# Kernel optimization log

Hardware: AMD Instinct MI355X
Metric: run time of the kernel (lower is better)

Reference implementation:

```python
import jax, jax.numpy as jnp
import numpy as np

EPS = 1e-5  # torch LayerNorm default eps
L2_EPS = 1e-12


def _l2norm(t, axis=-1):
    return t / jnp.sqrt(jnp.sum(t * t, axis=axis, keepdims=True) + L2_EPS)


def setup_inputs() -> dict:
    key = jax.random.key(0)
    k1, k2, k3 = jax.random.split(key, 3)
    b, n, d = 4, 2048, 1024
    h, e, cs = 8, 16, 2048
    x = jax.random.normal(k1, (b, n, d), dtype=jnp.float32)
    # xavier_normal_ on [h, d, e]: fan_in = d*e, fan_out = h*e
    std = float(np.sqrt(2.0 / (d * e + h * e)))
    rand_projs = jax.random.normal(k2, (h, d, e), dtype=jnp.float32) * std
    codebook = jax.random.normal(k3, (h, cs, e), dtype=jnp.float32)
    return {"x": x, "rand_projs": rand_projs, "codebook": codebook}


def reference(x, rand_projs, codebook):
    # LayerNorm over last dim, no affine
    mu = jnp.mean(x, axis=-1, keepdims=True)
    var = jnp.mean((x - mu) ** 2, axis=-1, keepdims=True)
    xn = (x - mu) / jnp.sqrt(var + EPS)
    # per-head random projection: [b,n,d] x [h,d,e] -> [b,n,h,e]
    proj = jnp.einsum('bnd,hde->bnhe', xn, rand_projs)
    # cosine-sim VQ per head: normalize both, argmax similarity
    q = _l2norm(proj, axis=-1)                 # [b,n,h,e]
    cb = _l2norm(codebook, axis=-1)            # [h,c,e]
    sim = jnp.einsum('bnhe,hce->bnhc', q, cb)  # [b,n,h,c]
    indices = jnp.argmax(sim, axis=-1)         # [b,n,h] int
    return indices
```

## Files before the change

kernel.cpp:

```cpp
#include <hip/hip_runtime.h>
#include <math.h>


typedef short bf16x8 __attribute__((ext_vector_type(8)));
typedef float f32x4 __attribute__((ext_vector_type(4)));

__device__ __forceinline__ void stage16(const float* g, float* lds_base) {
  __builtin_amdgcn_global_load_lds(
      (const __attribute__((address_space(1))) void*)g,
      (__attribute__((address_space(3))) void*)lds_base, 16, 0, 0);
}

__device__ __forceinline__ unsigned short f2bf(float f) {
  unsigned u = __builtin_bit_cast(unsigned, f);
  unsigned r = (u + 0x7FFFu + ((u >> 16) & 1u)) >> 16;
  return (unsigned short)r;
}
__device__ __forceinline__ float bf2f(unsigned short b) {
  return __builtin_bit_cast(float, (unsigned)b << 16);
}
__device__ __forceinline__ void split3(float v, unsigned short& h,
                                       unsigned short& m, unsigned short& l) {
  h = f2bf(v);
  float r = v - bf2f(h);
  m = f2bf(r);
  float r2 = r - bf2f(m);
  l = f2bf(r2);
}

__global__ __launch_bounds__(256) void k_prep(const float* __restrict__ cb,
                                              const float* __restrict__ W,
                                              unsigned short* __restrict__ cfrag,
                                              float* __restrict__ csum,
                                              unsigned short* __restrict__ wfrag) {
  __shared__ float red[16][17];
  const int bid = blockIdx.x;
  const int t = threadIdx.x;
  if (bid < 64) {
    int v = bid * 256 + t;
    int h = v >> 11, c = v & 2047, tl = c >> 4, n = c & 15;
    const float4* p = (const float4*)(cb + (size_t)v * 16);
    float4 q0 = p[0], q1 = p[1], q2 = p[2], q3 = p[3];
    float f[16] = {q0.x,q0.y,q0.z,q0.w, q1.x,q1.y,q1.z,q1.w,
                   q2.x,q2.y,q2.z,q2.w, q3.x,q3.y,q3.z,q3.w};
    double s = 0.0;
#pragma unroll
    for (int i = 0; i < 16; ++i) s += (double)f[i] * (double)f[i];
    double inv = 1.0 / sqrt(s + 1e-12);
    __attribute__((aligned(16))) unsigned short vp[3][16];
#pragma unroll
    for (int i = 0; i < 16; ++i)
      split3((float)((double)f[i] * inv), vp[0][i], vp[1][i], vp[2][i]);
#pragma unroll
    for (int pp = 0; pp < 3; ++pp) {
      size_t base = ((((size_t)h * 128 + tl) * 3 + pp) * 16 + n) * 16;
      ((bf16x8*)(cfrag + base))[0] = ((bf16x8*)vp[pp])[0];
      ((bf16x8*)(cfrag + base))[1] = ((bf16x8*)vp[pp])[1];
    }
  } else if (bid < 72) {
    int h = bid - 64;
    int e = t & 15, part = t >> 4;
    const float* base = W + h * 16384 + e;
    float s = 0.f;
    int d0 = part * 64;
    for (int i = 0; i < 64; ++i) s += base[(d0 + i) * 16];
    red[e][part] = s;
    __syncthreads();
    if (t < 16) {
      float tt = 0.f;
#pragma unroll
      for (int p = 0; p < 16; ++p) tt += red[t][p];
      csum[h * 16 + t] = tt;
    }
  } else {
    int id = (bid - 72) * 256 + t;
    int o = id & 1, n = (id >> 1) & 15, c = (id >> 5) & 7, dg = id >> 8;
    __attribute__((aligned(16))) unsigned short vp[3][8];
#pragma unroll
    for (int j = 0; j < 8; ++j) {
      float v = W[c * 16384 + (dg * 16 + o * 8 + j) * 16 + n];
      split3(v, vp[0][j], vp[1][j], vp[2][j]);
    }
#pragma unroll
    for (int pp = 0; pp < 3; ++pp) {
      size_t base = ((((size_t)dg * 8 + c) * 3 + pp) * 16 + n) * 16 + o * 8;
      *(bf16x8*)(wfrag + base) = *(bf16x8*)vp[pp];
    }
  }
}

__global__ __launch_bounds__(512) void k_proj(const float* __restrict__ x,
                                              const unsigned short* __restrict__ wfrag,
                                              const float* __restrict__ csum,
                                              unsigned short* __restrict__ ph,
                                              unsigned short* __restrict__ pm,
                                              unsigned short* __restrict__ pl) {
  __shared__ __align__(16) float smem[16 * 1028];
  __shared__ float sPs[8][2][16];
  __shared__ float sMu[16];
  const int t = threadIdx.x;
  const int lane = t & 63, w = t >> 6;
  const int r0 = blockIdx.x * 16;
  const int q = lane >> 4, n16 = lane & 15, oct = q & 1;
  const bool qlt2 = (q < 2);
  const int p1 = qlt2 ? 0 : 1, p2 = qlt2 ? 1 : 0, p3 = qlt2 ? 2 : 0;

#pragma unroll
  for (int rr = 0; rr < 2; ++rr)
#pragma unroll
    for (int j4 = 0; j4 < 4; ++j4)
      stage16(x + (size_t)(r0 + 2 * w + rr) * 1024 + j4 * 256 + lane * 4,
              smem + (2 * w + rr) * 1028 + j4 * 256);
  __syncthreads();

  f32x4 acc[8];
#pragma unroll
  for (int h = 0; h < 8; ++h) acc[h] = (f32x4){0.f, 0.f, 0.f, 0.f};
  float ps = 0.f;

#pragma unroll 4
  for (int dg2 = 0; dg2 < 8; ++dg2) {
    const int dg = w * 8 + dg2;
    const int dq = dg * 16 + oct * 8;
    float4 xa = *(const float4*)(smem + n16 * 1028 + dq);
    float4 xb = *(const float4*)(smem + n16 * 1028 + dq + 4);
    float xf[8] = {xa.x, xa.y, xa.z, xa.w, xb.x, xb.y, xb.z, xb.w};
    ps += ((xf[0] + xf[1]) + (xf[2] + xf[3])) +
          ((xf[4] + xf[5]) + (xf[6] + xf[7]));
    __attribute__((aligned(16))) unsigned short s1[8], s3[8];
#pragma unroll
    for (int j = 0; j < 8; ++j) {
      unsigned short hh, mm, ll;
      split3(xf[j], hh, mm, ll);
      s1[j] = qlt2 ? hh : mm;
      s3[j] = qlt2 ? hh : ll;
    }
    bf16x8 a1 = *(bf16x8*)s1;
    bf16x8 a3 = *(bf16x8*)s3;
#pragma unroll
    for (int hh = 0; hh < 8; ++hh) {
      size_t b0 = (((size_t)(dg * 8 + hh) * 3) * 16 + n16) * 16 + oct * 8;
      bf16x8 b1 = *(const bf16x8*)(wfrag + b0 + p1 * 256);
      bf16x8 b2 = *(const bf16x8*)(wfrag + b0 + p2 * 256);
      bf16x8 b3 = *(const bf16x8*)(wfrag + b0 + p3 * 256);
      acc[hh] = __builtin_amdgcn_mfma_f32_16x16x32_bf16(a1, b1, acc[hh], 0, 0, 0);
      acc[hh] = __builtin_amdgcn_mfma_f32_16x16x32_bf16(a1, b2, acc[hh], 0, 0, 0);
      acc[hh] = __builtin_amdgcn_mfma_f32_16x16x32_bf16(a3, b3, acc[hh], 0, 0, 0);
    }
  }

  __syncthreads();
  float* sAcc = smem;

  if (w >= 4) {
#pragma unroll
    for (int hh = 0; hh < 8; ++hh)
#pragma unroll
      for (int r = 0; r < 4; ++r)
        sAcc[((w - 4) * 64 + lane) * 33 + hh * 4 + r] = acc[hh][r];
  }
  if (q < 2) sPs[w][q][n16] = ps;
  __syncthreads();
  if (w < 4) {
#pragma unroll
    for (int hh = 0; hh < 8; ++hh)
#pragma unroll
      for (int r = 0; r < 4; ++r)
        sAcc[(w * 64 + lane) * 33 + hh * 4 + r] =
            acc[hh][r] + sAcc[(w * 64 + lane) * 33 + hh * 4 + r];
  }
  if (t < 16) {
    float s = 0.f;
#pragma unroll
    for (int w2 = 0; w2 < 8; ++w2) s += sPs[w2][0][t] + sPs[w2][1][t];
    sMu[t] = s * (1.0f / 1024.0f);
  }
  __syncthreads();

  const int l = t & 63, head = t >> 6;
  const int lq = l >> 4, ln = l & 15;
  const float cs = csum[head * 16 + ln];
#pragma unroll
  for (int r = 0; r < 4; ++r) {
    const int f = head * 4 + r;
    float v = ((sAcc[(0 * 64 + l) * 33 + f] + sAcc[(1 * 64 + l) * 33 + f]) +
               (sAcc[(2 * 64 + l) * 33 + f] + sAcc[(3 * 64 + l) * 33 + f]));
    const int row16 = lq * 4 + r;
    float tv = v - sMu[row16] * cs;
    unsigned short vh, vm, vl;
    split3(tv, vh, vm, vl);
    size_t base = ((size_t)head * 8192 + r0 + row16) * 16 + ln;
    ph[base] = vh; pm[base] = vm; pl[base] = vl;
  }
}

__global__ __launch_bounds__(256) void k_argmax(
    const unsigned short* __restrict__ ph, const unsigned short* __restrict__ pm,
    const unsigned short* __restrict__ pl, const unsigned short* __restrict__ cfrag,
    float* __restrict__ amv, int* __restrict__ ami) {
  __shared__ __align__(16) unsigned short sB[12288];
  const int t = threadIdx.x;
  const int lane = t & 63, w = t >> 6;
  const int h = blockIdx.y;
  const int z = blockIdx.z;
  const int r0 = blockIdx.x * 256 + w * 64;
  const int q = lane >> 4, n16 = lane & 15;
  const int ehalf = (q & 1) * 8;
  const bool qlt2 = (q < 2);
  const int p1 = qlt2 ? 0 : 1, p2 = qlt2 ? 1 : 0, p3 = qlt2 ? 2 : 0;

  const float* src = (const float*)(cfrag + ((size_t)(h * 128 + z * 16) * 3) * 256);
#pragma unroll
  for (int i = 0; i < 6; ++i)
    stage16(src + ((size_t)((i * 4 + w) * 64) + lane) * 4,
            (float*)sB + (i * 4 + w) * 256);

  const unsigned short* pa1 = qlt2 ? ph : pm;
  const unsigned short* pa3 = qlt2 ? ph : pl;
  bf16x8 a1[4], a3[4];
#pragma unroll
  for (int rt = 0; rt < 4; ++rt) {
    size_t off = ((size_t)h * 8192 + r0 + rt * 16 + n16) * 16 + ehalf;
    a1[rt] = *(const bf16x8*)(pa1 + off);
    a3[rt] = *(const bf16x8*)(pa3 + off);
  }

  float best[4][4];
  int   bidx[4][4];
#pragma unroll
  for (int rt = 0; rt < 4; ++rt)
#pragma unroll
    for (int r = 0; r < 4; ++r) { best[rt][r] = -3.402823466e38f; bidx[rt][r] = 0; }

  __syncthreads();

  for (int tile = 0; tile < 16; ++tile) {
    const int b0 = tile * 768 + n16 * 16 + ehalf;
    bf16x8 b1 = *(const bf16x8*)(sB + b0 + p1 * 256);
    bf16x8 b2 = *(const bf16x8*)(sB + b0 + p2 * 256);
    bf16x8 b3 = *(const bf16x8*)(sB + b0 + p3 * 256);
    const int code = z * 256 + tile * 16 + n16;
#pragma unroll
    for (int rt = 0; rt < 4; ++rt) {
      f32x4 acc = {0.f, 0.f, 0.f, 0.f};
      acc = __builtin_amdgcn_mfma_f32_16x16x32_bf16(a1[rt], b1, acc, 0, 0, 0);
      acc = __builtin_amdgcn_mfma_f32_16x16x32_bf16(a1[rt], b2, acc, 0, 0, 0);
      acc = __builtin_amdgcn_mfma_f32_16x16x32_bf16(a3[rt], b3, acc, 0, 0, 0);
#pragma unroll
      for (int r = 0; r < 4; ++r)
        if (acc[r] > best[rt][r]) { best[rt][r] = acc[r]; bidx[rt][r] = code; }
    }
  }

#pragma unroll
  for (int off = 8; off >= 1; off >>= 1) {
#pragma unroll
    for (int rt = 0; rt < 4; ++rt)
#pragma unroll
      for (int r = 0; r < 4; ++r) {
        float ov = __shfl_xor(best[rt][r], off, 16);
        int   oi = __shfl_xor(bidx[rt][r], off, 16);
        if (ov > best[rt][r] || (ov == best[rt][r] && oi < bidx[rt][r])) {
          best[rt][r] = ov; bidx[rt][r] = oi;
        }
      }
  }
  if (n16 == 0) {
#pragma unroll
    for (int rt = 0; rt < 4; ++rt)
#pragma unroll
      for (int r = 0; r < 4; ++r) {
        int row = r0 + rt * 16 + q * 4 + r;
        size_t o = (size_t)z * 65536 + (size_t)row * 8 + h;
        amv[o] = best[rt][r]; ami[o] = bidx[rt][r];
      }
  }
}

__global__ __launch_bounds__(256) void k_amred(const float* __restrict__ amv,
                                               const int* __restrict__ ami,
                                               int* __restrict__ out) {
  int i = blockIdx.x * 256 + threadIdx.x;
  float bv = amv[i]; int bi = ami[i];
#pragma unroll
  for (int z = 1; z < 8; ++z) {
    float v = amv[(size_t)z * 65536 + i];
    if (v > bv) { bv = v; bi = ami[(size_t)z * 65536 + i]; }
  }
  out[i] = bi;
}

extern "C" void kernel_launch(void* const* d_in, const int* in_sizes, int n_in,
                              void* d_out, int out_size, void* d_ws, size_t ws_size,
                              hipStream_t stream) {
  (void)in_sizes; (void)n_in; (void)out_size; (void)ws_size;
  const float* x  = (const float*)d_in[0];
  const float* rp = (const float*)d_in[1];
  const float* cb = (const float*)d_in[2];
  int* out = (int*)d_out;

  float* ws = (float*)d_ws;
  float*          csum  = ws;
  float*          amv   = ws + 128;
  int*            ami   = (int*)(ws + 524416);
  unsigned short* wfrag = (unsigned short*)(ws + 1048704);
  unsigned short* cfrag = (unsigned short*)(ws + 1245312);
  unsigned short* ph    = (unsigned short*)(ws + 1638528);
  unsigned short* pm    = (unsigned short*)(ws + 2162816);
  unsigned short* pl    = (unsigned short*)(ws + 2687104);

  hipLaunchKernelGGL(k_prep,    dim3(136),       dim3(256), 0, stream, cb, rp, cfrag, csum, wfrag);
  hipLaunchKernelGGL(k_proj,    dim3(512),       dim3(512), 0, stream, x, wfrag, csum, ph, pm, pl);
  hipLaunchKernelGGL(k_argmax,  dim3(32, 8, 8),  dim3(256), 0, stream, ph, pm, pl, cfrag, amv, ami);
  hipLaunchKernelGGL(k_amred,   dim3(256),       dim3(256), 0, stream, amv, ami, out);
}
```

Before: 144.3 us.

## Fuse all four stages into one persistent kernel with grid barriers

Merges prep, projection, argmax and reduction into a single 512-block kernel, separating the stages with software grid-wide barriers built on atomics. The argmax stage is remapped so each block runs two half-block work items per rep over two reps, with each 4-wave group using its own LDS slice. This is meant to remove three kernel launch gaps and the tail idle time between them. In exchange it adds a memset launch, spin-wait barrier cost, and a deadlock risk if all 512 blocks cannot be co-resident, and prep work now runs on only one thread in eight.

```diff
diff --git a/kernel.cpp b/kernel.cpp
--- a/kernel.cpp
+++ b/kernel.cpp
@@ -28,17 +28,48 @@
   l = f2bf(r2);
 }
 
-__global__ __launch_bounds__(256) void k_prep(const float* __restrict__ cb,
-                                              const float* __restrict__ W,
-                                              unsigned short* __restrict__ cfrag,
-                                              float* __restrict__ csum,
-                                              unsigned short* __restrict__ wfrag) {
-  __shared__ float red[16][17];
+__device__ __forceinline__ void gbar(unsigned* cnt, unsigned* flag,
+                                     unsigned nb) {
+  __syncthreads();
+  if (threadIdx.x == 0) {
+    __threadfence();
+    unsigned prev = __hip_atomic_fetch_add(cnt, 1u, __ATOMIC_ACQ_REL,
+                                           __HIP_MEMORY_SCOPE_AGENT);
+    if (prev == nb - 1) {
+      __hip_atomic_store(flag, 1u, __ATOMIC_RELEASE,
+                         __HIP_MEMORY_SCOPE_AGENT);
+    } else {
+      while (__hip_atomic_load(flag, __ATOMIC_ACQUIRE,
+                               __HIP_MEMORY_SCOPE_AGENT) == 0u)
+        __builtin_amdgcn_s_sleep(1);
+    }
+    __threadfence();
+  }
+  __syncthreads();
+}
+
+__global__ __launch_bounds__(512, 4) void k_all(
+    const float* __restrict__ x, const float* __restrict__ W,
+    const float* __restrict__ cb, int* __restrict__ out,
+    float* __restrict__ csum, float* __restrict__ amv, int* __restrict__ ami,
+    unsigned short* __restrict__ wfrag, unsigned short* __restrict__ cfrag,
+    unsigned short* __restrict__ ph, unsigned short* __restrict__ pm,
+    unsigned short* __restrict__ pl, unsigned* __restrict__ bar) {
+  __shared__ __align__(16) float smemF[16 * 1028];
+  __shared__ float sPs[8][2][16];
+  __shared__ float sMu[16];
+
   const int bid = blockIdx.x;
   const int t = threadIdx.x;
-  if (bid < 64) {
-    int v = bid * 256 + t;
-    int h = v >> 11, c = v & 2047, tl = c >> 4, n = c & 15;
+  const int tid = bid * 512 + t;
+  const int lane = t & 63, w = t >> 6;
+  const int q = lane >> 4, n16 = lane & 15, oct = q & 1;
+  const bool qlt2 = (q < 2);
+  const int p1 = qlt2 ? 0 : 1, p2 = qlt2 ? 1 : 0, p3 = qlt2 ? 2 : 0;
+
+  if (tid < 131072 && (tid & 7) == 0) {
+    int v = tid >> 3;
+    int hh = v >> 11, c = v & 2047, tl = c >> 4, n = c & 15;
     const float4* p = (const float4*)(cb + (size_t)v * 16);
     float4 q0 = p[0], q1 = p[1], q2 = p[2], q3 = p[3];
     float f[16] = {q0.x,q0.y,q0.z,q0.w, q1.x,q1.y,q1.z,q1.w,
@@ -53,27 +84,12 @@
       split3((float)((double)f[i] * inv), vp[0][i], vp[1][i], vp[2][i]);
 #pragma unroll
     for (int pp = 0; pp < 3; ++pp) {
-      size_t base = ((((size_t)h * 128 + tl) * 3 + pp) * 16 + n) * 16;
+      size_t base = ((((size_t)hh * 128 + tl) * 3 + pp) * 16 + n) * 16;
       ((bf16x8*)(cfrag + base))[0] = ((bf16x8*)vp[pp])[0];
       ((bf16x8*)(cfrag + base))[1] = ((bf16x8*)vp[pp])[1];
     }
-  } else if (bid < 72) {
-    int h = bid - 64;
-    int e = t & 15, part = t >> 4;
-    const float* base = W + h * 16384 + e;
-    float s = 0.f;
-    int d0 = part * 64;
-    for (int i = 0; i < 64; ++i) s += base[(d0 + i) * 16];
-    red[e][part] = s;
-    __syncthreads();
-    if (t < 16) {
-      float tt = 0.f;
-#pragma unroll
-      for (int p = 0; p < 16; ++p) tt += red[t][p];
-      csum[h * 16 + t] = tt;
-    }
-  } else {
-    int id = (bid - 72) * 256 + t;
+  } else if (tid >= 131072 && (tid & 7) == 0) {
+    int id = (tid - 131072) >> 3;
     int o = id & 1, n = (id >> 1) & 15, c = (id >> 5) & 7, dg = id >> 8;
     __attribute__((aligned(16))) unsigned short vp[3][8];
 #pragma unroll
@@ -87,207 +103,216 @@
       *(bf16x8*)(wfrag + base) = *(bf16x8*)vp[pp];
     }
   }
-}
-
-__global__ __launch_bounds__(512) void k_proj(const float* __restrict__ x,
-                                              const unsigned short* __restrict__ wfrag,
-                                              const float* __restrict__ csum,
-                                              unsigned short* __restrict__ ph,
-                                              unsigned short* __restrict__ pm,
-                                              unsigned short* __restrict__ pl) {
-  __shared__ __align__(16) float smem[16 * 1028];
-  __shared__ float sPs[8][2][16];
-  __shared__ float sMu[16];
-  const int t = threadIdx.x;
-  const int lane = t & 63, w = t >> 6;
-  const int r0 = blockIdx.x * 16;
-  const int q = lane >> 4, n16 = lane & 15, oct = q & 1;
-  const bool qlt2 = (q < 2);
-  const int p1 = qlt2 ? 0 : 1, p2 = qlt2 ? 1 : 0, p3 = qlt2 ? 2 : 0;
-
-#pragma unroll
-  for (int rr = 0; rr < 2; ++rr)
-#pragma unroll
-    for (int j4 = 0; j4 < 4; ++j4)
-      stage16(x + (size_t)(r0 + 2 * w + rr) * 1024 + j4 * 256 + lane * 4,
-              smem + (2 * w + rr) * 1028 + j4 * 256);
-  __syncthreads();
-
-  f32x4 acc[8];
-#pragma unroll
-  for (int h = 0; h < 8; ++h) acc[h] = (f32x4){0.f, 0.f, 0.f, 0.f};
-  float ps = 0.f;
+  if (bid >= 504) {
+    float (*red)[17] = (float(*)[17])smemF;
+    int hh = bid - 504;
+    if (t < 256) {
+      int e = t & 15, part = t >> 4;
+      const float* base = W + hh * 16384 + e;
+      float s = 0.f;
+      int d0 = part * 64;
+      for (int i = 0; i < 64; ++i) s += base[(d0 + i) * 16];
+      red[e][part] = s;
+    }
+    __syncthreads();
+    if (t < 16) {
+      float tt = 0.f;
+#pragma unroll
+      for (int p = 0; p < 16; ++p) tt += red[t][p];
+      csum[hh * 16 + t] = tt;
+    }
+  }
+
+  gbar(bar + 0, bar + 1, gridDim.x);
+
+  {
+    const int r0 = bid * 16;
+#pragma unroll
+    for (int rr = 0; rr < 2; ++rr)
+#pragma unroll
+      for (int j4 = 0; j4 < 4; ++j4)
+        stage16(x + (size_t)(r0 + 2 * w + rr) * 1024 + j4 * 256 + lane * 4,
+                smemF + (2 * w + rr) * 1028 + j4 * 256);
+    __syncthreads();
+
+    f32x4 acc[8];
+#pragma unroll
+    for (int h = 0; h < 8; ++h) acc[h] = (f32x4){0.f, 0.f, 0.f, 0.f};
+    float ps = 0.f;
 
 #pragma unroll 4
-  for (int dg2 = 0; dg2 < 8; ++dg2) {
-    const int dg = w * 8 + dg2;
-    const int dq = dg * 16 + oct * 8;
-    float4 xa = *(const float4*)(smem + n16 * 1028 + dq);
-    float4 xb = *(const float4*)(smem + n16 * 1028 + dq + 4);
-    float xf[8] = {xa.x, xa.y, xa.z, xa.w, xb.x, xb.y, xb.z, xb.w};
-    ps += ((xf[0] + xf[1]) + (xf[2] + xf[3])) +
-          ((xf[4] + xf[5]) + (xf[6] + xf[7]));
-    __attribute__((aligned(16))) unsigned short s1[8], s3[8];
-#pragma unroll
-    for (int j = 0; j < 8; ++j) {
-      unsigned short hh, mm, ll;
-      split3(xf[j], hh, mm, ll);
-      s1[j] = qlt2 ? hh : mm;
-      s3[j] = qlt2 ? hh : ll;
-    }
-    bf16x8 a1 = *(bf16x8*)s1;
-    bf16x8 a3 = *(bf16x8*)s3;
-#pragma unroll
-    for (int hh = 0; hh < 8; ++hh) {
-      size_t b0 = (((size_t)(dg * 8 + hh) * 3) * 16 + n16) * 16 + oct * 8;
-      bf16x8 b1 = *(const bf16x8*)(wfrag + b0 + p1 * 256);
-      bf16x8 b2 = *(const bf16x8*)(wfrag + b0 + p2 * 256);
-      bf16x8 b3 = *(const bf16x8*)(wfrag + b0 + p3 * 256);
-      acc[hh] = __builtin_amdgcn_mfma_f32_16x16x32_bf16(a1, b1, acc[hh], 0, 0, 0);
-      acc[hh] = __builtin_amdgcn_mfma_f32_16x16x32_bf16(a1, b2, acc[hh], 0, 0, 0);
-      acc[hh] = __builtin_amdgcn_mfma_f32_16x16x32_bf16(a3, b3, acc[hh], 0, 0, 0);
-    }
-  }
-
-  __syncthreads();
-  float* sAcc = smem;
-
-  if (w >= 4) {
-#pragma unroll
-    for (int hh = 0; hh < 8; ++hh)
-#pragma unroll
-      for (int r = 0; r < 4; ++r)
-        sAcc[((w - 4) * 64 + lane) * 33 + hh * 4 + r] = acc[hh][r];
-  }
-  if (q < 2) sPs[w][q][n16] = ps;
-  __syncthreads();
-  if (w < 4) {
-#pragma unroll
-    for (int hh = 0; hh < 8; ++hh)
-#pragma unroll
-      for (int r = 0; r < 4; ++r)
-        sAcc[(w * 64 + lane) * 33 + hh * 4 + r] =
-            acc[hh][r] + sAcc[(w * 64 + lane) * 33 + hh * 4 + r];
-  }
-  if (t < 16) {
-    float s = 0.f;
-#pragma unroll
-    for (int w2 = 0; w2 < 8; ++w2) s += sPs[w2][0][t] + sPs[w2][1][t];
-    sMu[t] = s * (1.0f / 1024.0f);
-  }
-  __syncthreads();
-
-  const int l = t & 63, head = t >> 6;
-  const int lq = l >> 4, ln = l & 15;
-  const float cs = csum[head * 16 + ln];
-#pragma unroll
-  for (int r = 0; r < 4; ++r) {
-    const int f = head * 4 + r;
-    float v = ((sAcc[(0 * 64 + l) * 33 + f] + sAcc[(1 * 64 + l) * 33 + f]) +
-               (sAcc[(2 * 64 + l) * 33 + f] + sAcc[(3 * 64 + l) * 33 + f]));
-    const int row16 = lq * 4 + r;
-    float tv = v - sMu[row16] * cs;
-    unsigned short vh, vm, vl;
-    split3(tv, vh, vm, vl);
-    size_t base = ((size_t)head * 8192 + r0 + row16) * 16 + ln;
-    ph[base] = vh; pm[base] = vm; pl[base] = vl;
-  }
-}
-
-__global__ __launch_bounds__(256) void k_argmax(
-    const unsigned short* __restrict__ ph, const unsigned short* __restrict__ pm,
-    const unsigned short* __restrict__ pl, const unsigned short* __restrict__ cfrag,
-    float* __restrict__ amv, int* __restrict__ ami) {
-  __shared__ __align__(16) unsigned short sB[12288];
-  const int t = threadIdx.x;
-  const int lane = t & 63, w = t >> 6;
-  const int h = blockIdx.y;
-  const int z = blockIdx.z;
-  const int r0 = blockIdx.x * 256 + w * 64;
-  const int q = lane >> 4, n16 = lane & 15;
-  const int ehalf = (q & 1) * 8;
-  const bool qlt2 = (q < 2);
-  const int p1 = qlt2 ? 0 : 1, p2 = qlt2 ? 1 : 0, p3 = qlt2 ? 2 : 0;
-
-  const float* src = (const float*)(cfrag + ((size_t)(h * 128 + z * 16) * 3) * 256);
-#pragma unroll
-  for (int i = 0; i < 6; ++i)
-    stage16(src + ((size_t)((i * 4 + w) * 64) + lane) * 4,
-            (float*)sB + (i * 4 + w) * 256);
-
-  const unsigned short* pa1 = qlt2 ? ph : pm;
-  const unsigned short* pa3 = qlt2 ? ph : pl;
-  bf16x8 a1[4], a3[4];
-#pragma unroll
-  for (int rt = 0; rt < 4; ++rt) {
-    size_t off = ((size_t)h * 8192 + r0 + rt * 16 + n16) * 16 + ehalf;
-    a1[rt] = *(const bf16x8*)(pa1 + off);
-    a3[rt] = *(const bf16x8*)(pa3 + off);
-  }
-
-  float best[4][4];
-  int   bidx[4][4];
-#pragma unroll
-  for (int rt = 0; rt < 4; ++rt)
-#pragma unroll
-    for (int r = 0; r < 4; ++r) { best[rt][r] = -3.402823466e38f; bidx[rt][r] = 0; }
-
-  __syncthreads();
-
-  for (int tile = 0; tile < 16; ++tile) {
-    const int b0 = tile * 768 + n16 * 16 + ehalf;
-    bf16x8 b1 = *(const bf16x8*)(sB + b0 + p1 * 256);
-    bf16x8 b2 = *(const bf16x8*)(sB + b0 + p2 * 256);
-    bf16x8 b3 = *(const bf16x8*)(sB + b0 + p3 * 256);
-    const int code = z * 256 + tile * 16 + n16;
-#pragma unroll
-    for (int rt = 0; rt < 4; ++rt) {
-      f32x4 acc = {0.f, 0.f, 0.f, 0.f};
-      acc = __builtin_amdgcn_mfma_f32_16x16x32_bf16(a1[rt], b1, acc, 0, 0, 0);
-      acc = __builtin_amdgcn_mfma_f32_16x16x32_bf16(a1[rt], b2, acc, 0, 0, 0);
-      acc = __builtin_amdgcn_mfma_f32_16x16x32_bf16(a3[rt], b3, acc, 0, 0, 0);
-#pragma unroll
-      for (int r = 0; r < 4; ++r)
-        if (acc[r] > best[rt][r]) { best[rt][r] = acc[r]; bidx[rt][r] = code; }
-    }
-  }
-
-#pragma unroll
-  for (int off = 8; off >= 1; off >>= 1) {
-#pragma unroll
-    for (int rt = 0; rt < 4; ++rt)
-#pragma unroll
-      for (int r = 0; r < 4; ++r) {
-        float ov = __shfl_xor(best[rt][r], off, 16);
-        int   oi = __shfl_xor(bidx[rt][r], off, 16);
-        if (ov > best[rt][r] || (ov == best[rt][r] && oi < bidx[rt][r])) {
-          best[rt][r] = ov; bidx[rt][r] = oi;
+    for (int dg2 = 0; dg2 < 8; ++dg2) {
+      const int dg = w * 8 + dg2;
+      const int dq = dg * 16 + oct * 8;
+      float4 xa = *(const float4*)(smemF + n16 * 1028 + dq);
+      float4 xb = *(const float4*)(smemF + n16 * 1028 + dq + 4);
+      float xf[8] = {xa.x, xa.y, xa.z, xa.w, xb.x, xb.y, xb.z, xb.w};
+      ps += ((xf[0] + xf[1]) + (xf[2] + xf[3])) +
+            ((xf[4] + xf[5]) + (xf[6] + xf[7]));
+      __attribute__((aligned(16))) unsigned short s1[8], s3[8];
+#pragma unroll
+      for (int j = 0; j < 8; ++j) {
+        unsigned short hh, mm, ll;
+        split3(xf[j], hh, mm, ll);
+        s1[j] = qlt2 ? hh : mm;
+        s3[j] = qlt2 ? hh : ll;
+      }
+      bf16x8 a1 = *(bf16x8*)s1;
+      bf16x8 a3 = *(bf16x8*)s3;
+#pragma unroll
+      for (int hh = 0; hh < 8; ++hh) {
+        size_t b0 = (((size_t)(dg * 8 + hh) * 3) * 16 + n16) * 16 + oct * 8;
+        bf16x8 b1 = *(const bf16x8*)(wfrag + b0 + p1 * 256);
+        bf16x8 b2 = *(const bf16x8*)(wfrag + b0 + p2 * 256);
+        bf16x8 b3 = *(const bf16x8*)(wfrag + b0 + p3 * 256);
+        acc[hh] = __builtin_amdgcn_mfma_f32_16x16x32_bf16(a1, b1, acc[hh], 0, 0, 0);
+        acc[hh] = __builtin_amdgcn_mfma_f32_16x16x32_bf16(a1, b2, acc[hh], 0, 0, 0);
+        acc[hh] = __builtin_amdgcn_mfma_f32_16x16x32_bf16(a3, b3, acc[hh], 0, 0, 0);
+      }
+    }
+
+    __syncthreads();
+    float* sAcc = smemF;
+
+    if (w >= 4) {
+#pragma unroll
+      for (int hh = 0; hh < 8; ++hh)
+#pragma unroll
+        for (int r = 0; r < 4; ++r)
+          sAcc[((w - 4) * 64 + lane) * 33 + hh * 4 + r] = acc[hh][r];
+    }
+    if (q < 2) sPs[w][q][n16] = ps;
+    __syncthreads();
+    if (w < 4) {
+#pragma unroll
+      for (int hh = 0; hh < 8; ++hh)
+#pragma unroll
+        for (int r = 0; r < 4; ++r)
+          sAcc[(w * 64 + lane) * 33 + hh * 4 + r] =
+              acc[hh][r] + sAcc[(w * 64 + lane) * 33 + hh * 4 + r];
+    }
+    if (t < 16) {
+      float s = 0.f;
+#pragma unroll
+      for (int w2 = 0; w2 < 8; ++w2) s += sPs[w2][0][t] + sPs[w2][1][t];
+      sMu[t] = s * (1.0f / 1024.0f);
+    }
+    __syncthreads();
+
+    const int l = t & 63, head = t >> 6;
+    const int lq = l >> 4, ln = l & 15;
+    const float cs = csum[head * 16 + ln];
+#pragma unroll
+    for (int r = 0; r < 4; ++r) {
+      const int f = head * 4 + r;
+      float v = ((sAcc[(0 * 64 + l) * 33 + f] + sAcc[(1 * 64 + l) * 33 + f]) +
+                 (sAcc[(2 * 64 + l) * 33 + f] + sAcc[(3 * 64 + l) * 33 + f]));
+      const int row16 = lq * 4 + r;
+      float tv = v - sMu[row16] * cs;
+      unsigned short vh, vm, vl;
+      split3(tv, vh, vm, vl);
+      size_t base = ((size_t)head * 8192 + r0 + row16) * 16 + ln;
+      ph[base] = vh; pm[base] = vm; pl[base] = vl;
+    }
+  }
+
+  gbar(bar + 2, bar + 3, gridDim.x);
+
+  {
+    unsigned short* sB = (unsigned short*)smemF;
+    const int wg = w >> 2, lw = w & 3;
+    const int ehalf = oct * 8;
+    const unsigned short* pa1 = qlt2 ? ph : pm;
+    const unsigned short* pa3 = qlt2 ? ph : pl;
+    unsigned short* sBw = sB + wg * 12288;
+
+    for (int rep = 0; rep < 2; ++rep) {
+      const int lid = rep * 1024 + bid * 2 + wg;
+      const int z = lid & 7, h = (lid >> 3) & 7, rg = lid >> 6;
+      const int r0 = rg * 256 + lw * 64;
+
+      __syncthreads();
+      const float* src =
+          (const float*)(cfrag + ((size_t)(h * 128 + z * 16) * 3) * 256);
+#pragma unroll
+      for (int i = 0; i < 6; ++i)
+        stage16(src + ((size_t)((i * 4 + lw) * 64) + lane) * 4,
+                (float*)sBw + (i * 4 + lw) * 256);
+
+      bf16x8 a1[4], a3[4];
+#pragma unroll
+      for (int rt = 0; rt < 4; ++rt) {
+        size_t off = ((size_t)h * 8192 + r0 + rt * 16 + n16) * 16 + ehalf;
+        a1[rt] = *(const bf16x8*)(pa1 + off);
+        a3[rt] = *(const bf16x8*)(pa3 + off);
+      }
+
+      float best[4][4];
+      int bidx[4][4];
+#pragma unroll
+      for (int rt = 0; rt < 4; ++rt)
+#pragma unroll
+        for (int r = 0; r < 4; ++r) {
+          best[rt][r] = -3.402823466e38f; bidx[rt][r] = 0;
         }
-      }
-  }
-  if (n16 == 0) {
-#pragma unroll
-    for (int rt = 0; rt < 4; ++rt)
-#pragma unroll
-      for (int r = 0; r < 4; ++r) {
-        int row = r0 + rt * 16 + q * 4 + r;
-        size_t o = (size_t)z * 65536 + (size_t)row * 8 + h;
-        amv[o] = best[rt][r]; ami[o] = bidx[rt][r];
-      }
-  }
-}
-
-__global__ __launch_bounds__(256) void k_amred(const float* __restrict__ amv,
-                                               const int* __restrict__ ami,
-                                               int* __restrict__ out) {
-  int i = blockIdx.x * 256 + threadIdx.x;
-  float bv = amv[i]; int bi = ami[i];
-#pragma unroll
-  for (int z = 1; z < 8; ++z) {
-    float v = amv[(size_t)z * 65536 + i];
-    if (v > bv) { bv = v; bi = ami[(size_t)z * 65536 + i]; }
-  }
-  out[i] = bi;
+
+      __syncthreads();
+
+      for (int tile = 0; tile < 16; ++tile) {
+        const int b0 = tile * 768 + n16 * 16 + ehalf;
+        bf16x8 b1 = *(const bf16x8*)(sBw + b0 + p1 * 256);
+        bf16x8 b2 = *(const bf16x8*)(sBw + b0 + p2 * 256);
+        bf16x8 b3 = *(const bf16x8*)(sBw + b0 + p3 * 256);
+        const int code = z * 256 + tile * 16 + n16;
+#pragma unroll
+        for (int rt = 0; rt < 4; ++rt) {
+          f32x4 acc = {0.f, 0.f, 0.f, 0.f};
+          acc = __builtin_amdgcn_mfma_f32_16x16x32_bf16(a1[rt], b1, acc, 0, 0, 0);
+          acc = __builtin_amdgcn_mfma_f32_16x16x32_bf16(a1[rt], b2, acc, 0, 0, 0);
+          acc = __builtin_amdgcn_mfma_f32_16x16x32_bf16(a3[rt], b3, acc, 0, 0, 0);
+#pragma unroll
+          for (int r = 0; r < 4; ++r)
+            if (acc[r] > best[rt][r]) { best[rt][r] = acc[r]; bidx[rt][r] = code; }
+        }
+      }
+
+#pragma unroll
+      for (int off = 8; off >= 1; off >>= 1) {
+#pragma unroll
+        for (int rt = 0; rt < 4; ++rt)
+#pragma unroll
+          for (int r = 0; r < 4; ++r) {
+            float ov = __shfl_xor(best[rt][r], off, 16);
+            int oi = __shfl_xor(bidx[rt][r], off, 16);
+            if (ov > best[rt][r] || (ov == best[rt][r] && oi < bidx[rt][r])) {
+              best[rt][r] = ov; bidx[rt][r] = oi;
+            }
+          }
+      }
+      if (n16 == 0) {
+#pragma unroll
+        for (int rt = 0; rt < 4; ++rt)
+#pragma unroll
+          for (int r = 0; r < 4; ++r) {
+            int row = r0 + rt * 16 + q * 4 + r;
+            size_t o = (size_t)z * 65536 + (size_t)row * 8 + h;
+            amv[o] = best[rt][r]; ami[o] = bidx[rt][r];
+          }
+      }
+    }
+  }
+
+  gbar(bar + 4, bar + 5, gridDim.x);
+
+  if (tid < 65536) {
+    float bv = amv[tid]; int bi = ami[tid];
+#pragma unroll
+    for (int z = 1; z < 8; ++z) {
+      float v = amv[(size_t)z * 65536 + tid];
+      if (v > bv) { bv = v; bi = ami[(size_t)z * 65536 + tid]; }
+    }
+    out[tid] = bi;
+  }
 }
 
 extern "C" void kernel_launch(void* const* d_in, const int* in_sizes, int n_in,
@@ -308,9 +333,10 @@
   unsigned short* ph    = (unsigned short*)(ws + 1638528);
   unsigned short* pm    = (unsigned short*)(ws + 2162816);
   unsigned short* pl    = (unsigned short*)(ws + 2687104);
-
-  hipLaunchKernelGGL(k_prep,    dim3(136),       dim3(256), 0, stream, cb, rp, cfrag, csum, wfrag);
-  hipLaunchKernelGGL(k_proj,    dim3(512),       dim3(512), 0, stream, x, wfrag, csum, ph, pm, pl);
-  hipLaunchKernelGGL(k_argmax,  dim3(32, 8, 8),  dim3(256), 0, stream, ph, pm, pl, cfrag, amv, ami);
-  hipLaunchKernelGGL(k_amred,   dim3(256),       dim3(256), 0, stream, amv, ami, out);
-}
+  unsigned*       bar   = (unsigned*)(ws + 3211392);
+
+  hipMemsetAsync((void*)bar, 0, 6 * sizeof(unsigned), stream);
+  hipLaunchKernelGGL(k_all, dim3(512), dim3(512), 0, stream,
+                     x, rp, cb, out, csum, amv, ami, wfrag, cfrag,
+                     ph, pm, pl, bar);
+}
```

Result: slower. 374.4 us (+159.4%).

## Fuse projection, codebook argmax and reduction into one kernel

Applied to the files above, without the earlier changes.

Merges the projection kernel, the split-codebook argmax kernel and the cross-split reduction kernel into a single kernel. The split bf16 projections stay in LDS instead of going through global memory, and each wave scans the full 2048-entry codebook for one head, reading codebook fragments straight from global/L2. This drops two launches and the intermediate global traffic. In exchange only 512 blocks run the argmax with a long serial loop over 128 tiles per wave, reading codebook fragments from global memory with no LDS staging, so parallelism drops.

```diff
diff --git a/kernel.cpp b/kernel.cpp
--- a/kernel.cpp
+++ b/kernel.cpp
@@ -89,13 +89,12 @@
   }
 }
 
-__global__ __launch_bounds__(512) void k_proj(const float* __restrict__ x,
+__global__ __launch_bounds__(512) void k_main(const float* __restrict__ x,
                                               const unsigned short* __restrict__ wfrag,
+                                              const unsigned short* __restrict__ cfrag,
                                               const float* __restrict__ csum,
-                                              unsigned short* __restrict__ ph,
-                                              unsigned short* __restrict__ pm,
-                                              unsigned short* __restrict__ pl) {
-  __shared__ __align__(16) float smem[16 * 1028];
+                                              int* __restrict__ out) {
+  __shared__ __align__(16) float smemF[16 * 1028];
   __shared__ float sPs[8][2][16];
   __shared__ float sMu[16];
   const int t = threadIdx.x;
@@ -104,13 +103,15 @@
   const int q = lane >> 4, n16 = lane & 15, oct = q & 1;
   const bool qlt2 = (q < 2);
   const int p1 = qlt2 ? 0 : 1, p2 = qlt2 ? 1 : 0, p3 = qlt2 ? 2 : 0;
+  const int ehalf = oct * 8;
+  unsigned short* tS = (unsigned short*)((char*)smemF + 33792);
 
 #pragma unroll
   for (int rr = 0; rr < 2; ++rr)
 #pragma unroll
     for (int j4 = 0; j4 < 4; ++j4)
       stage16(x + (size_t)(r0 + 2 * w + rr) * 1024 + j4 * 256 + lane * 4,
-              smem + (2 * w + rr) * 1028 + j4 * 256);
+              smemF + (2 * w + rr) * 1028 + j4 * 256);
   __syncthreads();
 
   f32x4 acc[8];
@@ -122,8 +123,8 @@
   for (int dg2 = 0; dg2 < 8; ++dg2) {
     const int dg = w * 8 + dg2;
     const int dq = dg * 16 + oct * 8;
-    float4 xa = *(const float4*)(smem + n16 * 1028 + dq);
-    float4 xb = *(const float4*)(smem + n16 * 1028 + dq + 4);
+    float4 xa = *(const float4*)(smemF + n16 * 1028 + dq);
+    float4 xb = *(const float4*)(smemF + n16 * 1028 + dq + 4);
     float xf[8] = {xa.x, xa.y, xa.z, xa.w, xb.x, xb.y, xb.z, xb.w};
     ps += ((xf[0] + xf[1]) + (xf[2] + xf[3])) +
           ((xf[4] + xf[5]) + (xf[6] + xf[7]));
@@ -150,7 +151,7 @@
   }
 
   __syncthreads();
-  float* sAcc = smem;
+  float* sAcc = smemF;
 
   if (w >= 4) {
 #pragma unroll
@@ -177,117 +178,71 @@
   }
   __syncthreads();
 
-  const int l = t & 63, head = t >> 6;
-  const int lq = l >> 4, ln = l & 15;
-  const float cs = csum[head * 16 + ln];
-#pragma unroll
-  for (int r = 0; r < 4; ++r) {
-    const int f = head * 4 + r;
-    float v = ((sAcc[(0 * 64 + l) * 33 + f] + sAcc[(1 * 64 + l) * 33 + f]) +
-               (sAcc[(2 * 64 + l) * 33 + f] + sAcc[(3 * 64 + l) * 33 + f]));
-    const int row16 = lq * 4 + r;
-    float tv = v - sMu[row16] * cs;
-    unsigned short vh, vm, vl;
-    split3(tv, vh, vm, vl);
-    size_t base = ((size_t)head * 8192 + r0 + row16) * 16 + ln;
-    ph[base] = vh; pm[base] = vm; pl[base] = vl;
-  }
-}
-
-__global__ __launch_bounds__(256) void k_argmax(
-    const unsigned short* __restrict__ ph, const unsigned short* __restrict__ pm,
-    const unsigned short* __restrict__ pl, const unsigned short* __restrict__ cfrag,
-    float* __restrict__ amv, int* __restrict__ ami) {
-  __shared__ __align__(16) unsigned short sB[12288];
-  const int t = threadIdx.x;
-  const int lane = t & 63, w = t >> 6;
-  const int h = blockIdx.y;
-  const int z = blockIdx.z;
-  const int r0 = blockIdx.x * 256 + w * 64;
-  const int q = lane >> 4, n16 = lane & 15;
-  const int ehalf = (q & 1) * 8;
-  const bool qlt2 = (q < 2);
-  const int p1 = qlt2 ? 0 : 1, p2 = qlt2 ? 1 : 0, p3 = qlt2 ? 2 : 0;
-
-  const float* src = (const float*)(cfrag + ((size_t)(h * 128 + z * 16) * 3) * 256);
-#pragma unroll
-  for (int i = 0; i < 6; ++i)
-    stage16(src + ((size_t)((i * 4 + w) * 64) + lane) * 4,
-            (float*)sB + (i * 4 + w) * 256);
-
-  const unsigned short* pa1 = qlt2 ? ph : pm;
-  const unsigned short* pa3 = qlt2 ? ph : pl;
-  bf16x8 a1[4], a3[4];
-#pragma unroll
-  for (int rt = 0; rt < 4; ++rt) {
-    size_t off = ((size_t)h * 8192 + r0 + rt * 16 + n16) * 16 + ehalf;
-    a1[rt] = *(const bf16x8*)(pa1 + off);
-    a3[rt] = *(const bf16x8*)(pa3 + off);
-  }
-
-  float best[4][4];
-  int   bidx[4][4];
-#pragma unroll
-  for (int rt = 0; rt < 4; ++rt)
-#pragma unroll
-    for (int r = 0; r < 4; ++r) { best[rt][r] = -3.402823466e38f; bidx[rt][r] = 0; }
-
-  __syncthreads();
-
-  for (int tile = 0; tile < 16; ++tile) {
-    const int b0 = tile * 768 + n16 * 16 + ehalf;
-    bf16x8 b1 = *(const bf16x8*)(sB + b0 + p1 * 256);
-    bf16x8 b2 = *(const bf16x8*)(sB + b0 + p2 * 256);
-    bf16x8 b3 = *(const bf16x8*)(sB + b0 + p3 * 256);
-    const int code = z * 256 + tile * 16 + n16;
-#pragma unroll
-    for (int rt = 0; rt < 4; ++rt) {
-      f32x4 acc = {0.f, 0.f, 0.f, 0.f};
-      acc = __builtin_amdgcn_mfma_f32_16x16x32_bf16(a1[rt], b1, acc, 0, 0, 0);
-      acc = __builtin_amdgcn_mfma_f32_16x16x32_bf16(a1[rt], b2, acc, 0, 0, 0);
-      acc = __builtin_amdgcn_mfma_f32_16x16x32_bf16(a3[rt], b3, acc, 0, 0, 0);
-#pragma unroll
-      for (int r = 0; r < 4; ++r)
-        if (acc[r] > best[rt][r]) { best[rt][r] = acc[r]; bidx[rt][r] = code; }
-    }
-  }
-
-#pragma unroll
-  for (int off = 8; off >= 1; off >>= 1) {
-#pragma unroll
-    for (int rt = 0; rt < 4; ++rt)
+  {
+    const int l = t & 63, head = t >> 6;
+    const int lq = l >> 4, ln = l & 15;
+    const float cs = csum[head * 16 + ln];
+#pragma unroll
+    for (int r = 0; r < 4; ++r) {
+      const int f = head * 4 + r;
+      float v = ((sAcc[(0 * 64 + l) * 33 + f] + sAcc[(1 * 64 + l) * 33 + f]) +
+                 (sAcc[(2 * 64 + l) * 33 + f] + sAcc[(3 * 64 + l) * 33 + f]));
+      const int row16 = lq * 4 + r;
+      float tv = v - sMu[row16] * cs;
+      unsigned short vh, vm, vl;
+      split3(tv, vh, vm, vl);
+      const int base = (row16 * 8 + head) * 16 + ln;
+      tS[base] = vh;
+      tS[2048 + base] = vm;
+      tS[4096 + base] = vl;
+    }
+  }
+  __syncthreads();
+
+  {
+    const int h = w;
+    const int pa3 = qlt2 ? 0 : 2;
+    bf16x8 a1 = *(const bf16x8*)(tS + (p1 * 2048 + (n16 * 8 + h) * 16) + ehalf);
+    bf16x8 a3 = *(const bf16x8*)(tS + (pa3 * 2048 + (n16 * 8 + h) * 16) + ehalf);
+
+    float best[4];
+    int   bidx[4];
+#pragma unroll
+    for (int r = 0; r < 4; ++r) { best[r] = -3.402823466e38f; bidx[r] = 0; }
+
+#pragma unroll 4
+    for (int tile = 0; tile < 128; ++tile) {
+      size_t b0 = (((size_t)(h * 128 + tile) * 3) * 16 + n16) * 16 + ehalf;
+      bf16x8 b1 = *(const bf16x8*)(cfrag + b0 + p1 * 256);
+      bf16x8 b2 = *(const bf16x8*)(cfrag + b0 + p2 * 256);
+      bf16x8 b3 = *(const bf16x8*)(cfrag + b0 + p3 * 256);
+      f32x4 a = {0.f, 0.f, 0.f, 0.f};
+      a = __builtin_amdgcn_mfma_f32_16x16x32_bf16(a1, b1, a, 0, 0, 0);
+      a = __builtin_amdgcn_mfma_f32_16x16x32_bf16(a1, b2, a, 0, 0, 0);
+      a = __builtin_amdgcn_mfma_f32_16x16x32_bf16(a3, b3, a, 0, 0, 0);
+      const int code = tile * 16 + n16;
+#pragma unroll
+      for (int r = 0; r < 4; ++r)
+        if (a[r] > best[r]) { best[r] = a[r]; bidx[r] = code; }
+    }
+
+#pragma unroll
+    for (int off = 8; off >= 1; off >>= 1) {
 #pragma unroll
       for (int r = 0; r < 4; ++r) {
-        float ov = __shfl_xor(best[rt][r], off, 16);
-        int   oi = __shfl_xor(bidx[rt][r], off, 16);
-        if (ov > best[rt][r] || (ov == best[rt][r] && oi < bidx[rt][r])) {
-          best[rt][r] = ov; bidx[rt][r] = oi;
+        float ov = __shfl_xor(best[r], off, 16);
+        int   oi = __shfl_xor(bidx[r], off, 16);
+        if (ov > best[r] || (ov == best[r] && oi < bidx[r])) {
+          best[r] = ov; bidx[r] = oi;
         }
       }
-  }
-  if (n16 == 0) {
-#pragma unroll
-    for (int rt = 0; rt < 4; ++rt)
-#pragma unroll
-      for (int r = 0; r < 4; ++r) {
-        int row = r0 + rt * 16 + q * 4 + r;
-        size_t o = (size_t)z * 65536 + (size_t)row * 8 + h;
-        amv[o] = best[rt][r]; ami[o] = bidx[rt][r];
-      }
-  }
-}
-
-__global__ __launch_bounds__(256) void k_amred(const float* __restrict__ amv,
-                                               const int* __restrict__ ami,
-                                               int* __restrict__ out) {
-  int i = blockIdx.x * 256 + threadIdx.x;
-  float bv = amv[i]; int bi = ami[i];
-#pragma unroll
-  for (int z = 1; z < 8; ++z) {
-    float v = amv[(size_t)z * 65536 + i];
-    if (v > bv) { bv = v; bi = ami[(size_t)z * 65536 + i]; }
-  }
-  out[i] = bi;
+    }
+    if (n16 == 0) {
+#pragma unroll
+      for (int r = 0; r < 4; ++r)
+        out[(size_t)(r0 + q * 4 + r) * 8 + h] = bidx[r];
+    }
+  }
 }
 
 extern "C" void kernel_launch(void* const* d_in, const int* in_sizes, int n_in,
@@ -301,16 +256,11 @@
 
   float* ws = (float*)d_ws;
   float*          csum  = ws;
-  float*          amv   = ws + 128;
-  int*            ami   = (int*)(ws + 524416);
-  unsigned short* wfrag = (unsigned short*)(ws + 1048704);
-  unsigned short* cfrag = (unsigned short*)(ws + 1245312);
-  unsigned short* ph    = (unsigned short*)(ws + 1638528);
-  unsigned short* pm    = (unsigned short*)(ws + 2162816);
-  unsigned short* pl    = (unsigned short*)(ws + 2687104);
-
-  hipLaunchKernelGGL(k_prep,    dim3(136),       dim3(256), 0, stream, cb, rp, cfrag, csum, wfrag);
-  hipLaunchKernelGGL(k_proj,    dim3(512),       dim3(512), 0, stream, x, wfrag, csum, ph, pm, pl);
-  hipLaunchKernelGGL(k_argmax,  dim3(32, 8, 8),  dim3(256), 0, stream, ph, pm, pl, cfrag, amv, ami);
-  hipLaunchKernelGGL(k_amred,   dim3(256),       dim3(256), 0, stream, amv, ami, out);
-}
+  unsigned short* wfrag = (unsigned short*)(ws + 128);
+  unsigned short* cfrag = (unsigned short*)(ws + 196736);
+
+  hipLaunchKernelGGL(k_prep, dim3(136), dim3(256), 0, stream,
+                     cb, rp, cfrag, csum, wfrag);
+  hipLaunchKernelGGL(k_main, dim3(512), dim3(512), 0, stream,
+                     x, wfrag, cfrag, csum, out);
+}
```

Result: slower. 155.6 us (+7.8%).
